# Kernel tuning notes

Hardware: AMD Instinct MI355X
Metric: run time of the kernel (lower is better)

Reference implementation:

```python
import jax, jax.numpy as jnp
import numpy as np

IN_F = 4096
OUT_F = 4096
NNZ = 1_600_000
BATCH = 512


def setup_inputs() -> dict:
    key = jax.random.key(0)
    k_x, k_w, k_b, k_r, k_c = jax.random.split(key, 5)
    x = jax.random.normal(k_x, (BATCH, IN_F), dtype=jnp.float32)
    weight1d = jax.random.normal(k_w, (NNZ,), dtype=jnp.float32) * 0.02
    bias = jax.random.normal(k_b, (OUT_F,), dtype=jnp.float32) * 0.02
    row_idx = jax.random.randint(k_r, (NNZ,), 0, OUT_F, dtype=jnp.int64 if jax.config.jax_enable_x64 else jnp.int32)
    col_idx = jax.random.randint(k_c, (NNZ,), 0, IN_F, dtype=jnp.int64 if jax.config.jax_enable_x64 else jnp.int32)
    return {
        "x": x,
        "weight1d": weight1d,
        "bias": bias,
        "row_idx": row_idx,
        "col_idx": col_idx,
        "in_f": IN_F,
        "out_f": OUT_F,
    }


def reference(x, weight1d, bias, row_idx, col_idx, in_f, out_f):
    # matching torch advanced-index assignment semantics up to duplicate ordering).
    W = jnp.zeros((out_f, in_f), dtype=weight1d.dtype).at[row_idx, col_idx].set(weight1d)
    # F.linear(x, W, bias) = x @ W.T + bias
    return x @ W.T + bias
```

## Files before the change

kernel.cpp:

```cpp
#include <hip/hip_runtime.h>
#include <hip/hip_bf16.h>

typedef unsigned short u16;
typedef unsigned long long u64;
typedef __attribute__((ext_vector_type(4))) float f32x4;
typedef __attribute__((ext_vector_type(8))) short bf16x8;

#define IN_F   4096
#define OUT_F  4096
#define BATCH  512

#define BM 128
#define BN 128
#define BK 64
#define KSPLIT 4
#define KC (IN_F / KSPLIT)
#define NSTEPS (KC / BK)

#define NXCD    8
#define NB      256
#define CHUNK   2048
#define LCAP    24
#define SEGCAP  2048
#define RCAP    640
#define GOVFCAP (1024*1024)
#define OVF2CAP (128*1024)
#define NCTR    (NXCD * NB + 2)

__device__ inline u16 f2bf(float f) {
    __hip_bfloat16 h = __float2bfloat16(f);
    u16 u; __builtin_memcpy(&u, &h, 2); return u;
}

__global__ __launch_bounds__(256) void conv_x(const float* __restrict__ x,
                                              u16* __restrict__ xbf,
                                              int* __restrict__ ctrs) {
    const int tid = threadIdx.x;
    if (blockIdx.x == 0) {
        for (int j = tid; j < NCTR; j += 256) ctrs[j] = 0;
    }
    int i = blockIdx.x * 256 + tid;
    float4 v = ((const float4*)x)[i];
    ushort4 o;
    o.x = f2bf(v.x); o.y = f2bf(v.y); o.z = f2bf(v.z); o.w = f2bf(v.w);
    ((ushort4*)xbf)[i] = o;
}

__global__ __launch_bounds__(256) void bucket_scatter(const int* __restrict__ row,
                                                      const int* __restrict__ col,
                                                      const float* __restrict__ w,
                                                      int* __restrict__ gcur,
                                                      u64* __restrict__ bins,
                                                      int* __restrict__ govf_cnt,
                                                      u64* __restrict__ govf, int nnz) {
    __shared__ u64 lbin[NB][LCAP];
    __shared__ int lcur[NB];
    const int xcd = __builtin_amdgcn_s_getreg(20 | (3 << 11)) & (NXCD - 1);
    const int tid = threadIdx.x;
    lcur[tid] = 0;
    __syncthreads();

    int base = blockIdx.x * CHUNK + tid * 8;
    if (base + 8 <= nnz) {
        int4 r0 = ((const int4*)(row + base))[0];
        int4 r1 = ((const int4*)(row + base))[1];
        int4 c0 = ((const int4*)(col + base))[0];
        int4 c1 = ((const int4*)(col + base))[1];
        float4 w0 = ((const float4*)(w + base))[0];
        float4 w1 = ((const float4*)(w + base))[1];
        int rs[8] = {r0.x, r0.y, r0.z, r0.w, r1.x, r1.y, r1.z, r1.w};
        int cs[8] = {c0.x, c0.y, c0.z, c0.w, c1.x, c1.y, c1.z, c1.w};
        float wsv[8] = {w0.x, w0.y, w0.z, w0.w, w1.x, w1.y, w1.z, w1.w};
#pragma unroll
        for (int j = 0; j < 8; j++) {
            int rr = rs[j], cc = cs[j], i = base + j;
            u64 wb = (u64)f2bf(wsv[j]);
            int bk = rr >> 4;
            int p = atomicAdd(&lcur[bk], 1);
            if (p < LCAP) {
                lbin[bk][p] = ((u64)i << 32) | ((u64)(rr & 15) << 28) | ((u64)cc << 16) | wb;
            } else {
                int o = atomicAdd(govf_cnt, 1);
                if (o < GOVFCAP) govf[o] = ((u64)i << 40) | ((u64)rr << 28) | ((u64)cc << 16) | wb;
            }
        }
    } else {
        int e = nnz < base + 8 ? nnz : base + 8;
        for (int i = base; i < e; i++) {
            int rr = row[i], cc = col[i];
            u64 wb = (u64)f2bf(w[i]);
            int bk = rr >> 4;
            int p = atomicAdd(&lcur[bk], 1);
            if (p < LCAP) {
                lbin[bk][p] = ((u64)i << 32) | ((u64)(rr & 15) << 28) | ((u64)cc << 16) | wb;
            } else {
                int o = atomicAdd(govf_cnt, 1);
                if (o < GOVFCAP) govf[o] = ((u64)i << 40) | ((u64)rr << 28) | ((u64)cc << 16) | wb;
            }
        }
    }
    __syncthreads();

    int cnt = lcur[tid];
    if (cnt > LCAP) cnt = LCAP;
    if (cnt > 0) {
        int gb = (xcd << 8) | tid;
        int b0 = atomicAdd(&gcur[gb], cnt);
        u64* seg = bins + (size_t)gb * SEGCAP;
        for (int k = 0; k < cnt; k++) {
            u64 e = lbin[tid][k];
            int p = b0 + k;
            if (p < SEGCAP) {
                seg[p] = e;
            } else {
                int rr = (tid << 4) | ((int)(e >> 28) & 15);
                int o = atomicAdd(govf_cnt, 1);
                if (o < GOVFCAP) govf[o] = ((e >> 32) << 40) | ((u64)rr << 28) | (e & 0x0FFFFFFF);
            }
        }
    }
}

__global__ __launch_bounds__(256) void split_bucket(const int* __restrict__ gcur,
                                                    const u64* __restrict__ bins,
                                                    const int* __restrict__ govf_cnt,
                                                    const u64* __restrict__ govf,
                                                    u64* __restrict__ rowbins,
                                                    int* __restrict__ rowcnt,
                                                    int* __restrict__ ovf2_cnt,
                                                    u64* __restrict__ ovf2) {
    __shared__ u64 lists[16][RCAP];
    __shared__ int lcur[16];
    const int bucket = blockIdx.x;
    const int tid = threadIdx.x;
    if (tid < 16) lcur[tid] = 0;
    __syncthreads();

#pragma unroll
    for (int xcd = 0; xcd < NXCD; xcd++) {
        int gb = (xcd << 8) | bucket;
        int cnt = gcur[gb];
        if (cnt > SEGCAP) cnt = SEGCAP;
        const u64* seg = bins + (size_t)gb * SEGCAP;
        for (int k = tid; k < cnt; k += 256) {
            u64 e = seg[k];
            int rl = (int)(e >> 28) & 15;
            int p = atomicAdd(&lcur[rl], 1);
            if (p < RCAP) lists[rl][p] = e;
            else {
                int rr = (bucket << 4) | rl;
                int o = atomicAdd(ovf2_cnt, 1);
                if (o < OVF2CAP) ovf2[o] = ((e >> 32) << 40) | ((u64)rr << 28) | (e & 0x0FFFFFFF);
            }
        }
    }
    int ovfn = *govf_cnt;
    if (ovfn > GOVFCAP) ovfn = GOVFCAP;
    for (int k = tid; k < ovfn; k += 256) {
        u64 e = govf[k];
        int rr = (int)(e >> 28) & 4095;
        if ((rr >> 4) == bucket) {
            u64 e2 = ((e >> 40) << 32) | ((u64)(rr & 15) << 28) | (e & 0x0FFFFFFF);
            int rl = rr & 15;
            int p = atomicAdd(&lcur[rl], 1);
            if (p < RCAP) lists[rl][p] = e2;
            else { int o = atomicAdd(ovf2_cnt, 1); if (o < OVF2CAP) ovf2[o] = ((e2 >> 32) << 40) | ((u64)rr << 28) | (e2 & 0x0FFFFFFF); }
        }
    }
    __syncthreads();

    for (int rl = 0; rl < 16; rl++) {
        int cnt = lcur[rl];
        if (cnt > RCAP) cnt = RCAP;
        int rowg = (bucket << 4) | rl;
        u64* dst = rowbins + (size_t)rowg * RCAP;
        for (int k = tid; k < cnt; k += 256) dst[k] = lists[rl][k];
        if (tid == 0) rowcnt[rowg] = cnt;
    }
}

__global__ __launch_bounds__(256) void build_row2(const u64* __restrict__ rowbins,
                                                  const int* __restrict__ rowcnt,
                                                  const int* __restrict__ ovf2_cnt,
                                                  const u64* __restrict__ ovf2,
                                                  u16* __restrict__ Wbf) {
    __shared__ u64 aux[IN_F];
    const int rowg = blockIdx.x;
    const int tid = threadIdx.x;

#pragma unroll
    for (int j = 0; j < IN_F / 256 / 2; j++)
        ((ulonglong2*)aux)[tid * 8 + j] = (ulonglong2){0ull, 0ull};
    __syncthreads();

    int cnt = rowcnt[rowg];
    const u64* seg = rowbins + (size_t)rowg * RCAP;
    for (int k = tid; k < cnt; k += 256) {
        u64 e = seg[k];
        atomicMax(&aux[(int)(e >> 16) & 4095], ((e >> 32) << 16) | (e & 0xFFFF));
    }
    int o2 = *ovf2_cnt;
    if (o2 > OVF2CAP) o2 = OVF2CAP;
    for (int k = tid; k < o2; k += 256) {
        u64 e = ovf2[k];
        if (((int)(e >> 28) & 4095) == rowg)
            atomicMax(&aux[(int)(e >> 16) & 4095], ((e >> 40) << 16) | (e & 0xFFFF));
    }
    __syncthreads();

    int base = tid * 16;
    ushort4 o[4];
#pragma unroll
    for (int j = 0; j < 16; j++)
        ((u16*)o)[j] = (u16)(aux[base + j] & 0xFFFF);
    uint4* dst = (uint4*)(Wbf + (size_t)rowg * IN_F + base);
    dst[0] = ((const uint4*)o)[0];
    dst[1] = ((const uint4*)o)[1];
}

__global__ __launch_bounds__(256) void gemm_part(const u16* __restrict__ A,
                                                 const u16* __restrict__ B,
                                                 u16* __restrict__ part) {
    __shared__ u16 As[2][BM * BK];
    __shared__ u16 Bs[2][BN * BK];
    const int L   = blockIdx.x;
    const int xx  = L & 7;
    const int rst = L >> 3;
    const int m   = rst & 3;
    const int g   = ((rst >> 2) << 3) | xx;
    const int n   = g & 31;
    const int kc  = g >> 5;
    const int m0  = m * BM;
    const int n0  = n * BN;
    const int kt0 = kc * KC;

    const int tid  = threadIdx.x;
    const int lane = tid & 63;
    const int wave = tid >> 6;
    const int wm = wave >> 1, wn = wave & 1;
    const int r15 = lane & 15, khi = lane >> 4;

    const u16* srcA[4]; const u16* srcB[4]; int dstO[4];
#pragma unroll
    for (int it = 0; it < 4; it++) {
        int o = tid * 16 + it * 4096;
        int rr = o >> 7, lblk = (o >> 4) & 7;
        srcA[it] = A + (size_t)(m0 + rr) * IN_F + kt0 + ((lblk ^ (rr & 7)) << 3);
        srcB[it] = B + (size_t)(n0 + rr) * IN_F + kt0 + ((lblk ^ (rr & 7)) << 3);
        dstO[it] = o >> 1;
    }

#define STAGE(buf, kk)                                                               \
    do {                                                                             \
        _Pragma("unroll")                                                            \
        for (int it = 0; it < 4; it++)                                               \
            __builtin_amdgcn_global_load_lds(                                        \
                (const __attribute__((address_space(1))) void*)(srcA[it] + (kk)),    \
                (__attribute__((address_space(3))) void*)(&As[buf][dstO[it]]),       \
                16, 0, 0);                                                           \
        _Pragma("unroll")                                                            \
        for (int it = 0; it < 4; it++)                                               \
            __builtin_amdgcn_global_load_lds(                                        \
                (const __attribute__((address_space(1))) void*)(srcB[it] + (kk)),    \
                (__attribute__((address_space(3))) void*)(&Bs[buf][dstO[it]]),       \
                16, 0, 0);                                                           \
    } while (0)

    f32x4 acc[4][4];
#pragma unroll
    for (int mi = 0; mi < 4; mi++)
#pragma unroll
        for (int nj = 0; nj < 4; nj++) acc[mi][nj] = (f32x4){0.f, 0.f, 0.f, 0.f};

    STAGE(0, 0);

    for (int t = 0; t < NSTEPS; ++t) {
        const int cur = t & 1;
        if (t + 1 < NSTEPS) {
            STAGE(cur ^ 1, (t + 1) * BK);
            asm volatile("s_waitcnt vmcnt(8)" ::: "memory");
        } else {
            asm volatile("s_waitcnt vmcnt(0)" ::: "memory");
        }
        __builtin_amdgcn_s_barrier();

        const char* as = (const char*)&As[cur][0];
        const char* bs = (const char*)&Bs[cur][0];
#pragma unroll
        for (int ks = 0; ks < 2; ks++) {
            bf16x8 a[4], b[4];
#pragma unroll
            for (int mi = 0; mi < 4; mi++) {
                int rowi = wm * 64 + mi * 16 + r15;
                a[mi] = *(const bf16x8*)(as + rowi * 128 + (((ks * 4 + khi) ^ (rowi & 7)) << 4));
            }
#pragma unroll
            for (int nj = 0; nj < 4; nj++) {
                int rowi = wn * 64 + nj * 16 + r15;
                b[nj] = *(const bf16x8*)(bs + rowi * 128 + (((ks * 4 + khi) ^ (rowi & 7)) << 4));
            }
#pragma unroll
            for (int mi = 0; mi < 4; mi++)
#pragma unroll
                for (int nj = 0; nj < 4; nj++)
                    acc[mi][nj] = __builtin_amdgcn_mfma_f32_16x16x32_bf16(a[mi], b[nj], acc[mi][nj], 0, 0, 0);
        }
        __builtin_amdgcn_s_barrier();
    }
#undef STAGE

    u16* P = part + (size_t)kc * BATCH * OUT_F;
#pragma unroll
    for (int nj = 0; nj < 4; nj++) {
        int colg = n0 + wn * 64 + nj * 16 + r15;
#pragma unroll
        for (int mi = 0; mi < 4; mi++) {
#pragma unroll
            for (int j = 0; j < 4; j++) {
                int rowg = m0 + wm * 64 + mi * 16 + khi * 4 + j;
                P[(size_t)rowg * OUT_F + colg] = f2bf(acc[mi][nj][j]);
            }
        }
    }
}

__global__ __launch_bounds__(256) void reduce_bias(const u16* __restrict__ part,
                                                   const float* __restrict__ bias,
                                                   float* __restrict__ y) {
    int i = blockIdx.x * 256 + threadIdx.x;
    const size_t S = (size_t)BATCH * OUT_F / 8;
    float s[8];
#pragma unroll
    for (int e = 0; e < 8; e++) s[e] = 0.f;
#pragma unroll
    for (int k = 0; k < KSPLIT; k++) {
        ushort4 v0 = ((const ushort4*)part)[(i + k * S) * 2 + 0];
        ushort4 v1 = ((const ushort4*)part)[(i + k * S) * 2 + 1];
        unsigned vv[8] = {v0.x, v0.y, v0.z, v0.w, v1.x, v1.y, v1.z, v1.w};
#pragma unroll
        for (int e = 0; e < 8; e++) {
            unsigned u = vv[e] << 16;
            float f; __builtin_memcpy(&f, &u, 4);
            s[e] += f;
        }
    }
    int col = (i * 8) & (OUT_F - 1);
    f32x4 b0 = *(const f32x4*)&bias[col];
    f32x4 b1 = *(const f32x4*)&bias[col + 4];
    f32x4 o0 = {s[0] + b0[0], s[1] + b0[1], s[2] + b0[2], s[3] + b0[3]};
    f32x4 o1 = {s[4] + b1[0], s[5] + b1[1], s[6] + b1[2], s[7] + b1[3]};
    ((f32x4*)y)[i * 2 + 0] = o0;
    ((f32x4*)y)[i * 2 + 1] = o1;
}

extern "C" void kernel_launch(void* const* d_in, const int* in_sizes, int n_in,
                              void* d_out, int out_size, void* d_ws, size_t ws_size,
                              hipStream_t stream) {
    const float* x    = (const float*)d_in[0];
    const float* w1d  = (const float*)d_in[1];
    const float* bias = (const float*)d_in[2];
    const int*   row  = (const int*)d_in[3];
    const int*   col  = (const int*)d_in[4];
    const int nnz = in_sizes[1];

    char* ws        = (char*)d_ws;
    u64*  bins      = (u64*)ws;
    u16*  part      = (u16*)ws;
    int*  gcur      = (int*)(ws + ((size_t)32 << 20));
    int*  govf_cnt  = gcur + NXCD * NB;
    int*  ovf2_cnt  = govf_cnt + 1;
    u64*  govf      = (u64*)(ws + ((size_t)33 << 20));
    u64*  rowbins   = (u64*)(ws + ((size_t)41 << 20));
    int*  rowcnt    = (int*)(ws + ((size_t)61 << 20));
    u64*  ovf2      = (u64*)(ws + ((size_t)62 << 20));
    u16*  Wbf       = (u16*)(ws + ((size_t)64 << 20));
    u16*  xbf       = (u16*)(ws + ((size_t)96 << 20));
    float* y        = (float*)d_out;

    conv_x<<<(BATCH * IN_F / 4) / 256, 256, 0, stream>>>(x, xbf, gcur);
    int nblk = (nnz + CHUNK - 1) / CHUNK;
    bucket_scatter<<<nblk, 256, 0, stream>>>(row, col, w1d, gcur, bins, govf_cnt, govf, nnz);
    split_bucket<<<NB, 256, 0, stream>>>(gcur, bins, govf_cnt, govf, rowbins, rowcnt, ovf2_cnt, ovf2);
    build_row2<<<OUT_F, 256, 0, stream>>>(rowbins, rowcnt, ovf2_cnt, ovf2, Wbf);
    gemm_part<<<512, 256, 0, stream>>>(xbf, Wbf, part);
    reduce_bias<<<(BATCH * OUT_F / 8) / 256, 256, 0, stream>>>(part, bias, y);
}
```

Measured before the change: 100.1 us.

## Fuse bucket splitting and dense row building into one kernel

Merges split_bucket and build_row2 so each block sorts its bucket into per-row LDS lists and then scatters each of its 16 rows into an LDS row buffer, writing the bf16 weight rows directly. This drops the rowbins/ovf2 global round-trip and one kernel launch. Per-row overflow now goes to a small LDS stash capped at 256 entries instead of a large global buffer, so extreme row skew could silently drop entries. Row building runs serially within 256 large-LDS blocks rather than across 4096 blocks, which lowers parallelism and occupancy.

```diff
diff --git a/kernel.cpp b/kernel.cpp
--- a/kernel.cpp
+++ b/kernel.cpp
@@ -23,8 +23,8 @@
 #define LCAP    24
 #define SEGCAP  2048
 #define RCAP    640
+#define SCAP2   256
 #define GOVFCAP (1024*1024)
-#define OVF2CAP (128*1024)
 #define NCTR    (NXCD * NB + 2)
 
 __device__ inline u16 f2bf(float f) {
@@ -121,19 +121,20 @@
     }
 }
 
-__global__ __launch_bounds__(256) void split_bucket(const int* __restrict__ gcur,
-                                                    const u64* __restrict__ bins,
-                                                    const int* __restrict__ govf_cnt,
-                                                    const u64* __restrict__ govf,
-                                                    u64* __restrict__ rowbins,
-                                                    int* __restrict__ rowcnt,
-                                                    int* __restrict__ ovf2_cnt,
-                                                    u64* __restrict__ ovf2) {
+__global__ __launch_bounds__(256) void split_build(const int* __restrict__ gcur,
+                                                   const u64* __restrict__ bins,
+                                                   const int* __restrict__ govf_cnt,
+                                                   const u64* __restrict__ govf,
+                                                   u16* __restrict__ Wbf) {
     __shared__ u64 lists[16][RCAP];
+    __shared__ u64 stash[SCAP2];
+    __shared__ u64 aux[IN_F];
     __shared__ int lcur[16];
+    __shared__ int scnt;
     const int bucket = blockIdx.x;
     const int tid = threadIdx.x;
     if (tid < 16) lcur[tid] = 0;
+    if (tid == 0) scnt = 0;
     __syncthreads();
 
 #pragma unroll
@@ -147,11 +148,7 @@
             int rl = (int)(e >> 28) & 15;
             int p = atomicAdd(&lcur[rl], 1);
             if (p < RCAP) lists[rl][p] = e;
-            else {
-                int rr = (bucket << 4) | rl;
-                int o = atomicAdd(ovf2_cnt, 1);
-                if (o < OVF2CAP) ovf2[o] = ((e >> 32) << 40) | ((u64)rr << 28) | (e & 0x0FFFFFFF);
-            }
+            else { int s = atomicAdd(&scnt, 1); if (s < SCAP2) stash[s] = e; }
         }
     }
     int ovfn = *govf_cnt;
@@ -164,58 +161,42 @@
             int rl = rr & 15;
             int p = atomicAdd(&lcur[rl], 1);
             if (p < RCAP) lists[rl][p] = e2;
-            else { int o = atomicAdd(ovf2_cnt, 1); if (o < OVF2CAP) ovf2[o] = ((e2 >> 32) << 40) | ((u64)rr << 28) | (e2 & 0x0FFFFFFF); }
+            else { int s = atomicAdd(&scnt, 1); if (s < SCAP2) stash[s] = e2; }
         }
     }
     __syncthreads();
+    const int sn = scnt > SCAP2 ? SCAP2 : scnt;
 
     for (int rl = 0; rl < 16; rl++) {
+#pragma unroll
+        for (int j = 0; j < 8; j++)
+            ((ulonglong2*)aux)[tid * 8 + j] = (ulonglong2){0ull, 0ull};
+        __syncthreads();
+
         int cnt = lcur[rl];
         if (cnt > RCAP) cnt = RCAP;
+        for (int k = tid; k < cnt; k += 256) {
+            u64 e = lists[rl][k];
+            atomicMax(&aux[(int)(e >> 16) & 4095], ((e >> 32) << 16) | (e & 0xFFFF));
+        }
+        for (int k = tid; k < sn; k += 256) {
+            u64 e = stash[k];
+            if (((int)(e >> 28) & 15) == rl)
+                atomicMax(&aux[(int)(e >> 16) & 4095], ((e >> 32) << 16) | (e & 0xFFFF));
+        }
+        __syncthreads();
+
         int rowg = (bucket << 4) | rl;
-        u64* dst = rowbins + (size_t)rowg * RCAP;
-        for (int k = tid; k < cnt; k += 256) dst[k] = lists[rl][k];
-        if (tid == 0) rowcnt[rowg] = cnt;
-    }
-}
-
-__global__ __launch_bounds__(256) void build_row2(const u64* __restrict__ rowbins,
-                                                  const int* __restrict__ rowcnt,
-                                                  const int* __restrict__ ovf2_cnt,
-                                                  const u64* __restrict__ ovf2,
-                                                  u16* __restrict__ Wbf) {
-    __shared__ u64 aux[IN_F];
-    const int rowg = blockIdx.x;
-    const int tid = threadIdx.x;
-
-#pragma unroll
-    for (int j = 0; j < IN_F / 256 / 2; j++)
-        ((ulonglong2*)aux)[tid * 8 + j] = (ulonglong2){0ull, 0ull};
-    __syncthreads();
-
-    int cnt = rowcnt[rowg];
-    const u64* seg = rowbins + (size_t)rowg * RCAP;
-    for (int k = tid; k < cnt; k += 256) {
-        u64 e = seg[k];
-        atomicMax(&aux[(int)(e >> 16) & 4095], ((e >> 32) << 16) | (e & 0xFFFF));
-    }
-    int o2 = *ovf2_cnt;
-    if (o2 > OVF2CAP) o2 = OVF2CAP;
-    for (int k = tid; k < o2; k += 256) {
-        u64 e = ovf2[k];
-        if (((int)(e >> 28) & 4095) == rowg)
-            atomicMax(&aux[(int)(e >> 16) & 4095], ((e >> 40) << 16) | (e & 0xFFFF));
-    }
-    __syncthreads();
-
-    int base = tid * 16;
-    ushort4 o[4];
-#pragma unroll
-    for (int j = 0; j < 16; j++)
-        ((u16*)o)[j] = (u16)(aux[base + j] & 0xFFFF);
-    uint4* dst = (uint4*)(Wbf + (size_t)rowg * IN_F + base);
-    dst[0] = ((const uint4*)o)[0];
-    dst[1] = ((const uint4*)o)[1];
+        int base = tid * 16;
+        ushort4 o[4];
+#pragma unroll
+        for (int j = 0; j < 16; j++)
+            ((u16*)o)[j] = (u16)(aux[base + j] & 0xFFFF);
+        uint4* dst = (uint4*)(Wbf + (size_t)rowg * IN_F + base);
+        dst[0] = ((const uint4*)o)[0];
+        dst[1] = ((const uint4*)o)[1];
+        __syncthreads();
+    }
 }
 
 __global__ __launch_bounds__(256) void gemm_part(const u16* __restrict__ A,
@@ -368,11 +349,7 @@
     u16*  part      = (u16*)ws;
     int*  gcur      = (int*)(ws + ((size_t)32 << 20));
     int*  govf_cnt  = gcur + NXCD * NB;
-    int*  ovf2_cnt  = govf_cnt + 1;
     u64*  govf      = (u64*)(ws + ((size_t)33 << 20));
-    u64*  rowbins   = (u64*)(ws + ((size_t)41 << 20));
-    int*  rowcnt    = (int*)(ws + ((size_t)61 << 20));
-    u64*  ovf2      = (u64*)(ws + ((size_t)62 << 20));
     u16*  Wbf       = (u16*)(ws + ((size_t)64 << 20));
     u16*  xbf       = (u16*)(ws + ((size_t)96 << 20));
     float* y        = (float*)d_out;
@@ -380,8 +357,7 @@
     conv_x<<<(BATCH * IN_F / 4) / 256, 256, 0, stream>>>(x, xbf, gcur);
     int nblk = (nnz + CHUNK - 1) / CHUNK;
     bucket_scatter<<<nblk, 256, 0, stream>>>(row, col, w1d, gcur, bins, govf_cnt, govf, nnz);
-    split_bucket<<<NB, 256, 0, stream>>>(gcur, bins, govf_cnt, govf, rowbins, rowcnt, ovf2_cnt, ovf2);
-    build_row2<<<OUT_F, 256, 0, stream>>>(rowbins, rowcnt, ovf2_cnt, ovf2, Wbf);
+    split_build<<<NB, 256, 0, stream>>>(gcur, bins, govf_cnt, govf, Wbf);
     gemm_part<<<512, 256, 0, stream>>>(xbf, Wbf, part);
     reduce_bias<<<(BATCH * OUT_F / 8) / 256, 256, 0, stream>>>(part, bias, y);
 }
```

Result: no change. 98.70 us (-1.4%).
